# Kernel tuning notes

Hardware: AMD Instinct MI355X
Metric: run time of the kernel (lower is better)

## Reference

```python
import jax, jax.numpy as jnp
import numpy as np

# NVFP4 (e2m1) 4-bit codebook: sign bit in the high position of the nibble
_NVFP4_CODE = jnp.array([0.0, 0.5, 1.0, 1.5, 2.0, 3.0, 4.0, 6.0,
                         -0.0, -0.5, -1.0, -1.5, -2.0, -3.0, -4.0, -6.0],
                        dtype=jnp.float32)

M = 4096          # tokens (batch*seq)
K = 4096          # in_features
N_NVFP4 = 2048
N_FP8 = 1024
N_FP16 = 1024
N = N_NVFP4 + N_FP8 + N_FP16  # out_features
BLOCK = 16        # NVFP4 scale block size along K


def setup_inputs() -> dict:
    key = jax.random.key(0)
    ks = jax.random.split(key, 8)
    x = jax.random.normal(ks[0], (M, K), dtype=jnp.float32)
    nvfp4_idx = jax.random.randint(ks[1], (N_NVFP4, K), 0, 16, dtype=jnp.int32)
    nvfp4_scales = jax.random.uniform(ks[2], (N_NVFP4, K // BLOCK), dtype=jnp.float32) * 0.5 + 0.05
    nvfp4_global_scale = jax.random.uniform(ks[3], (1,), dtype=jnp.float32) * 0.5 + 0.5
    w_fp8 = jax.random.normal(ks[4], (N_FP8, K), dtype=jnp.float32)
    fp8_scale = jax.random.uniform(ks[5], (1,), dtype=jnp.float32) * 0.1 + 0.01
    w_fp16 = jax.random.normal(ks[6], (N_FP16, K), dtype=jnp.float32) * 0.02
    bias = jax.random.normal(ks[7], (N,), dtype=jnp.float32) * 0.01
    inv_perm = jax.random.permutation(jax.random.fold_in(key, 99), N).astype(jnp.int64)
    return {"x": x, "nvfp4_idx": nvfp4_idx, "nvfp4_scales": nvfp4_scales,
            "nvfp4_global_scale": nvfp4_global_scale, "w_fp8": w_fp8,
            "fp8_scale": fp8_scale, "w_fp16": w_fp16, "bias": bias,
            "inv_perm": inv_perm}


def reference(x, nvfp4_idx, nvfp4_scales, nvfp4_global_scale,
              w_fp8, fp8_scale, w_fp16, bias, inv_perm):
    # --- NVFP4 group: dequantize 4-bit codes with per-16-block fp8 scales + global scale
    codes = _NVFP4_CODE[nvfp4_idx]                                   # [n_nvfp4, K]
    scales_full = jnp.repeat(nvfp4_scales, BLOCK, axis=1)            # [n_nvfp4, K]
    w_nvfp4 = codes * scales_full * nvfp4_global_scale[0]            # [n_nvfp4, K]
    y_nvfp4 = jnp.einsum('mk,nk->mn', x, w_nvfp4)                    # [M, n_nvfp4]
    # --- FP8 group: per-tensor scale
    y_fp8 = jnp.einsum('mk,nk->mn', x, w_fp8) * fp8_scale[0]         # [M, n_fp8]
    # --- FP16 group: plain GEMM
    y_fp16 = jnp.einsum('mk,nk->mn', x, w_fp16)                      # [M, n_fp16]
    # --- Reassemble in original channel order via inverse permutation
    y_grouped = jnp.concatenate([y_nvfp4, y_fp8, y_fp16], axis=-1)   # [M, N]
    y = jnp.take(y_grouped, inv_perm, axis=-1)
    return y + bias
```

## Files before the change

kernel.cpp:

```cpp
#include <hip/hip_runtime.h>

#define M_DIM 4096
#define N_DIM 4096
#define K_DIM 4096

typedef float f32x4 __attribute__((ext_vector_type(4)));
typedef __bf16 bf16x8 __attribute__((ext_vector_type(8)));

__device__ __forceinline__ unsigned short f2b(float f) {
    unsigned int u = __float_as_uint(f);
    u += 0x7fffu + ((u >> 16) & 1u);
    return (unsigned short)(u >> 16);
}

__device__ __constant__ float NVFP4_CODE[16] = {
    0.0f, 0.5f, 1.0f, 1.5f, 2.0f, 3.0f, 4.0f, 6.0f,
    -0.0f, -0.5f, -1.0f, -1.5f, -2.0f, -3.0f, -4.0f, -6.0f
};

__global__ __launch_bounds__(256) void cvt_x_kernel(const float* __restrict__ x,
                                                    unsigned short* __restrict__ xb) {
    size_t i = ((size_t)blockIdx.x * 256 + threadIdx.x) * 8;
    float4 a = *(const float4*)(x + i);
    float4 b = *(const float4*)(x + i + 4);
    union { unsigned short h[8]; uint4 u; } o;
    o.h[0] = f2b(a.x); o.h[1] = f2b(a.y); o.h[2] = f2b(a.z); o.h[3] = f2b(a.w);
    o.h[4] = f2b(b.x); o.h[5] = f2b(b.y); o.h[6] = f2b(b.z); o.h[7] = f2b(b.w);
    *(uint4*)(xb + i) = o.u;
}

__global__ __launch_bounds__(256) void build_w_kernel(
        const int* __restrict__ idx4, const float* __restrict__ sc4,
        const float* __restrict__ gs4, const float* __restrict__ w8,
        const float* __restrict__ s8, const float* __restrict__ w16,
        const int* __restrict__ iperm, unsigned short* __restrict__ W) {
    const int j = blockIdx.x;
    const int t = threadIdx.x;
    const int g = iperm[j];
    const int k0 = t * 16;
    union { unsigned short h[16]; uint4 u[2]; } o;

    if (g < 2048) {
        const float s = sc4[(size_t)g * (K_DIM / 16) + t] * gs4[0];
        const int4* ip = (const int4*)(idx4 + (size_t)g * K_DIM + k0);
#pragma unroll
        for (int b = 0; b < 4; ++b) {
            int4 v = ip[b];
            o.h[b * 4 + 0] = f2b(NVFP4_CODE[v.x & 15] * s);
            o.h[b * 4 + 1] = f2b(NVFP4_CODE[v.y & 15] * s);
            o.h[b * 4 + 2] = f2b(NVFP4_CODE[v.z & 15] * s);
            o.h[b * 4 + 3] = f2b(NVFP4_CODE[v.w & 15] * s);
        }
    } else if (g < 3072) {
        const float s = s8[0];
        const float4* wp = (const float4*)(w8 + (size_t)(g - 2048) * K_DIM + k0);
#pragma unroll
        for (int b = 0; b < 4; ++b) {
            float4 v = wp[b];
            o.h[b * 4 + 0] = f2b(v.x * s); o.h[b * 4 + 1] = f2b(v.y * s);
            o.h[b * 4 + 2] = f2b(v.z * s); o.h[b * 4 + 3] = f2b(v.w * s);
        }
    } else {
        const float4* wp = (const float4*)(w16 + (size_t)(g - 3072) * K_DIM + k0);
#pragma unroll
        for (int b = 0; b < 4; ++b) {
            float4 v = wp[b];
            o.h[b * 4 + 0] = f2b(v.x); o.h[b * 4 + 1] = f2b(v.y);
            o.h[b * 4 + 2] = f2b(v.z); o.h[b * 4 + 3] = f2b(v.w);
        }
    }
    uint4* dst = (uint4*)(W + (size_t)j * K_DIM + k0);
    dst[0] = o.u[0];
    dst[1] = o.u[1];
}

#define GLOAD_LDS16(g, l)                                                     \
    __builtin_amdgcn_global_load_lds(                                         \
        (const __attribute__((address_space(1))) void*)(unsigned long long)(g),\
        (__attribute__((address_space(3))) void*)(unsigned int)(unsigned long long)(l), \
        16, 0, 0)

__global__ __launch_bounds__(256) void gemm_kernel(
        const unsigned short* __restrict__ X, const unsigned short* __restrict__ W,
        const float* __restrict__ bias, float* __restrict__ C) {
    __shared__ __align__(16) unsigned short As[128 * 32];
    __shared__ __align__(16) unsigned short Bs[128 * 32];

    const int tid  = threadIdx.x;
    const int wave = tid >> 6;
    const int lane = tid & 63;
    const int quad = lane >> 4;
    const int l16  = lane & 15;
    const int wr   = wave >> 1;
    const int wc   = wave & 1;
    const int m0 = blockIdx.y * 128;
    const int n0 = blockIdx.x * 128;

    const int c0 = wave * 64 + lane;
    const int c1 = c0 + 256;
    const int rA0 = c0 >> 2, kc0 = (c0 & 3) * 8;
    const int rA1 = c1 >> 2, kc1 = (c1 & 3) * 8;

    const unsigned short* Xa0 = X + (size_t)(m0 + rA0) * K_DIM + kc0;
    const unsigned short* Xa1 = X + (size_t)(m0 + rA1) * K_DIM + kc1;
    const unsigned short* Wb0 = W + (size_t)(n0 + rA0) * K_DIM + kc0;
    const unsigned short* Wb1 = W + (size_t)(n0 + rA1) * K_DIM + kc1;

    f32x4 acc[4][4] = {};

    for (int kt = 0; kt < K_DIM / 32; ++kt) {
        const int k0 = kt * 32;
        GLOAD_LDS16(Xa0 + k0, &As[c0 * 8]);
        GLOAD_LDS16(Xa1 + k0, &As[c1 * 8]);
        GLOAD_LDS16(Wb0 + k0, &Bs[c0 * 8]);
        GLOAD_LDS16(Wb1 + k0, &Bs[c1 * 8]);
        __syncthreads();

        bf16x8 af[4], bq[4];
#pragma unroll
        for (int i = 0; i < 4; ++i)
            af[i] = *(const bf16x8*)&As[(wr * 64 + i * 16 + l16) * 32 + quad * 8];
#pragma unroll
        for (int jj = 0; jj < 4; ++jj)
            bq[jj] = *(const bf16x8*)&Bs[(wc * 64 + jj * 16 + l16) * 32 + quad * 8];

#pragma unroll
        for (int i = 0; i < 4; ++i)
#pragma unroll
            for (int jj = 0; jj < 4; ++jj)
                acc[i][jj] = __builtin_amdgcn_mfma_f32_16x16x32_bf16(
                    af[i], bq[jj], acc[i][jj], 0, 0, 0);

        __syncthreads();
    }

#pragma unroll
    for (int jj = 0; jj < 4; ++jj) {
        const int col = n0 + wc * 64 + jj * 16 + l16;
        const float bv = bias[col];
#pragma unroll
        for (int i = 0; i < 4; ++i) {
            const int rowb = m0 + wr * 64 + i * 16 + quad * 4;
#pragma unroll
            for (int r = 0; r < 4; ++r)
                C[(size_t)(rowb + r) * N_DIM + col] = acc[i][jj][r] + bv;
        }
    }
}

extern "C" void kernel_launch(void* const* d_in, const int* in_sizes, int n_in,
                              void* d_out, int out_size, void* d_ws, size_t ws_size,
                              hipStream_t stream) {
    const float* x            = (const float*)d_in[0];
    const int*   nvfp4_idx    = (const int*)d_in[1];
    const float* nvfp4_scales = (const float*)d_in[2];
    const float* gscale       = (const float*)d_in[3];
    const float* w_fp8        = (const float*)d_in[4];
    const float* fp8_scale    = (const float*)d_in[5];
    const float* w_fp16       = (const float*)d_in[6];
    const float* bias         = (const float*)d_in[7];
    const int*   inv_perm     = (const int*)d_in[8];
    float* out = (float*)d_out;

    unsigned short* xb = (unsigned short*)d_ws;
    unsigned short* wb = xb + (size_t)M_DIM * K_DIM;

    cvt_x_kernel<<<(M_DIM * (size_t)K_DIM) / (256 * 8), 256, 0, stream>>>(x, xb);
    build_w_kernel<<<N_DIM, 256, 0, stream>>>(nvfp4_idx, nvfp4_scales, gscale,
                                              w_fp8, fp8_scale, w_fp16, inv_perm, wb);
    gemm_kernel<<<dim3(N_DIM / 128, M_DIM / 128), 256, 0, stream>>>(xb, wb, bias, out);
}
```

Before: 362.3 us.

## Merge prep kernels, decode NVFP4 arithmetically, and group-swizzle GEMM tiles

Fuses the x-to-bf16 conversion and the weight build into one launch, which removes one kernel launch and the gap between the two. Replaces the constant-memory NVFP4 codebook lookup with bit manipulation that builds the float directly. Remaps the GEMM's 1D block index into groups of 8 M-tiles so that neighbouring blocks share X and W tiles in L2. The changes are independent, and the fused prep kernel now has divergent block roles.

```diff
diff --git a/kernel.cpp b/kernel.cpp
--- a/kernel.cpp
+++ b/kernel.cpp
@@ -13,28 +13,33 @@
     return (unsigned short)(u >> 16);
 }
 
-__device__ __constant__ float NVFP4_CODE[16] = {
-    0.0f, 0.5f, 1.0f, 1.5f, 2.0f, 3.0f, 4.0f, 6.0f,
-    -0.0f, -0.5f, -1.0f, -1.5f, -2.0f, -3.0f, -4.0f, -6.0f
-};
-
-__global__ __launch_bounds__(256) void cvt_x_kernel(const float* __restrict__ x,
-                                                    unsigned short* __restrict__ xb) {
-    size_t i = ((size_t)blockIdx.x * 256 + threadIdx.x) * 8;
-    float4 a = *(const float4*)(x + i);
-    float4 b = *(const float4*)(x + i + 4);
-    union { unsigned short h[8]; uint4 u; } o;
-    o.h[0] = f2b(a.x); o.h[1] = f2b(a.y); o.h[2] = f2b(a.z); o.h[3] = f2b(a.w);
-    o.h[4] = f2b(b.x); o.h[5] = f2b(b.y); o.h[6] = f2b(b.z); o.h[7] = f2b(b.w);
-    *(uint4*)(xb + i) = o.u;
+__device__ __forceinline__ float nvfp4_decode(int n) {
+    unsigned m = (unsigned)n & 7u;
+    unsigned e = m >> 1, f = m & 1u;
+    unsigned bits = (m >= 2u) ? (((126u + e) << 23) | (f << 22))
+                              : (m * 0x3f000000u);
+    bits |= ((unsigned)n & 8u) << 28;
+    return __uint_as_float(bits);
 }
 
-__global__ __launch_bounds__(256) void build_w_kernel(
+__global__ __launch_bounds__(256) void prep_kernel(
+        const float* __restrict__ x, unsigned short* __restrict__ xb,
         const int* __restrict__ idx4, const float* __restrict__ sc4,
         const float* __restrict__ gs4, const float* __restrict__ w8,
         const float* __restrict__ s8, const float* __restrict__ w16,
         const int* __restrict__ iperm, unsigned short* __restrict__ W) {
-    const int j = blockIdx.x;
+    const int b = blockIdx.x;
+    if (b < 8192) {
+        size_t i = ((size_t)b * 256 + threadIdx.x) * 8;
+        float4 a0 = *(const float4*)(x + i);
+        float4 a1 = *(const float4*)(x + i + 4);
+        union { unsigned short h[8]; uint4 u; } o;
+        o.h[0] = f2b(a0.x); o.h[1] = f2b(a0.y); o.h[2] = f2b(a0.z); o.h[3] = f2b(a0.w);
+        o.h[4] = f2b(a1.x); o.h[5] = f2b(a1.y); o.h[6] = f2b(a1.z); o.h[7] = f2b(a1.w);
+        *(uint4*)(xb + i) = o.u;
+        return;
+    }
+    const int j = b - 8192;
     const int t = threadIdx.x;
     const int g = iperm[j];
     const int k0 = t * 16;
@@ -44,29 +49,29 @@
         const float s = sc4[(size_t)g * (K_DIM / 16) + t] * gs4[0];
         const int4* ip = (const int4*)(idx4 + (size_t)g * K_DIM + k0);
 #pragma unroll
-        for (int b = 0; b < 4; ++b) {
-            int4 v = ip[b];
-            o.h[b * 4 + 0] = f2b(NVFP4_CODE[v.x & 15] * s);
-            o.h[b * 4 + 1] = f2b(NVFP4_CODE[v.y & 15] * s);
-            o.h[b * 4 + 2] = f2b(NVFP4_CODE[v.z & 15] * s);
-            o.h[b * 4 + 3] = f2b(NVFP4_CODE[v.w & 15] * s);
+        for (int bb = 0; bb < 4; ++bb) {
+            int4 v = ip[bb];
+            o.h[bb * 4 + 0] = f2b(nvfp4_decode(v.x) * s);
+            o.h[bb * 4 + 1] = f2b(nvfp4_decode(v.y) * s);
+            o.h[bb * 4 + 2] = f2b(nvfp4_decode(v.z) * s);
+            o.h[bb * 4 + 3] = f2b(nvfp4_decode(v.w) * s);
         }
     } else if (g < 3072) {
         const float s = s8[0];
         const float4* wp = (const float4*)(w8 + (size_t)(g - 2048) * K_DIM + k0);
 #pragma unroll
-        for (int b = 0; b < 4; ++b) {
-            float4 v = wp[b];
-            o.h[b * 4 + 0] = f2b(v.x * s); o.h[b * 4 + 1] = f2b(v.y * s);
-            o.h[b * 4 + 2] = f2b(v.z * s); o.h[b * 4 + 3] = f2b(v.w * s);
+        for (int bb = 0; bb < 4; ++bb) {
+            float4 v = wp[bb];
+            o.h[bb * 4 + 0] = f2b(v.x * s); o.h[bb * 4 + 1] = f2b(v.y * s);
+            o.h[bb * 4 + 2] = f2b(v.z * s); o.h[bb * 4 + 3] = f2b(v.w * s);
         }
     } else {
         const float4* wp = (const float4*)(w16 + (size_t)(g - 3072) * K_DIM + k0);
 #pragma unroll
-        for (int b = 0; b < 4; ++b) {
-            float4 v = wp[b];
-            o.h[b * 4 + 0] = f2b(v.x); o.h[b * 4 + 1] = f2b(v.y);
-            o.h[b * 4 + 2] = f2b(v.z); o.h[b * 4 + 3] = f2b(v.w);
+        for (int bb = 0; bb < 4; ++bb) {
+            float4 v = wp[bb];
+            o.h[bb * 4 + 0] = f2b(v.x); o.h[bb * 4 + 1] = f2b(v.y);
+            o.h[bb * 4 + 2] = f2b(v.z); o.h[bb * 4 + 3] = f2b(v.w);
         }
     }
     uint4* dst = (uint4*)(W + (size_t)j * K_DIM + k0);
@@ -86,6 +91,16 @@
     __shared__ __align__(16) unsigned short As[128 * 32];
     __shared__ __align__(16) unsigned short Bs[128 * 32];
 
+    const int pid = blockIdx.x;
+    const int GROUP = 8;
+    const int group_sz = GROUP * (N_DIM / 128);
+    const int grp = pid / group_sz;
+    const int rem = pid % group_sz;
+    const int bm = grp * GROUP + (rem % GROUP);
+    const int bn = rem / GROUP;
+    const int m0 = bm * 128;
+    const int n0 = bn * 128;
+
     const int tid  = threadIdx.x;
     const int wave = tid >> 6;
     const int lane = tid & 63;
@@ -93,8 +108,6 @@
     const int l16  = lane & 15;
     const int wr   = wave >> 1;
     const int wc   = wave & 1;
-    const int m0 = blockIdx.y * 128;
-    const int n0 = blockIdx.x * 128;
 
     const int c0 = wave * 64 + lane;
     const int c1 = c0 + 256;
@@ -165,8 +178,8 @@
     unsigned short* xb = (unsigned short*)d_ws;
     unsigned short* wb = xb + (size_t)M_DIM * K_DIM;
 
-    cvt_x_kernel<<<(M_DIM * (size_t)K_DIM) / (256 * 8), 256, 0, stream>>>(x, xb);
-    build_w_kernel<<<N_DIM, 256, 0, stream>>>(nvfp4_idx, nvfp4_scales, gscale,
-                                              w_fp8, fp8_scale, w_fp16, inv_perm, wb);
-    gemm_kernel<<<dim3(N_DIM / 128, M_DIM / 128), 256, 0, stream>>>(xb, wb, bias, out);
+    prep_kernel<<<8192 + 4096, 256, 0, stream>>>(x, xb, nvfp4_idx, nvfp4_scales,
+                                                 gscale, w_fp8, fp8_scale, w_fp16,
+                                                 inv_perm, wb);
+    gemm_kernel<<<(M_DIM / 128) * (N_DIM / 128), 256, 0, stream>>>(xb, wb, bias, out);
 }
```

Result: no change. 365.3 us (+0.8%).
